# Kernel tuning notes

Measured on AMD Instinct MI355X. Metric: run time of the kernel, lower is better.

The kernel has to match this reference:

```python
import jax, jax.numpy as jnp
import numpy as np

D_MODEL = 512; DEPTH = 4; HEADS = 8; BUCKET = 256; N_HASHES = 4
INPUT_DIM = 32; SEQ = 2 * BUCKET; BATCH = 16; DH = D_MODEL // HEADS
N_BUCKETS = SEQ // BUCKET  # 2 (seq_len is forced to 2*bucket_size by pos_encoding)
SELF_ATTN_VALUE = -5e4  # TOKEN_SELF_ATTN_VALUE in reformer_pytorch


def layer_norm(x, g, b, eps=1e-5):
    m = jnp.mean(x, -1, keepdims=True)
    v = jnp.mean((x - m) ** 2, -1, keepdims=True)
    return (x - m) / jnp.sqrt(v + eps) * g + b


def look_one_back(x):
    # each chunk also attends to the previous chunk (circularly)
    prev = jnp.concatenate([x[:, -1:], x[:, :-1]], axis=1)
    return jnp.concatenate([x, prev], axis=2)


def lsh_attention(qk, v, rot):
    # qk, v: (B*H, T, DH); rot: (DH, N_HASHES, N_BUCKETS//2). Shared-QK LSH attention.
    B, T, d = qk.shape
    rotated = jnp.einsum('btf,fhi->bhti', qk, rot)                  # (B, nh, T, nb/2)
    rotated = jnp.concatenate([rotated, -rotated], axis=-1)        # (B, nh, T, nb)
    buckets = jnp.argmax(rotated, axis=-1)                          # (B, nh, T)
    offsets = (jnp.arange(N_HASHES) * N_BUCKETS)[None, :, None]
    buckets = (buckets + offsets).reshape(B, N_HASHES * T)
    ticker = jnp.arange(N_HASHES * T) % T
    bkt = T * buckets + ticker[None, :]                             # unique sort keys
    sticker = jnp.argsort(bkt, axis=-1)
    undo = jnp.argsort(sticker, axis=-1)
    st = sticker % T
    sqk = jnp.take_along_axis(qk, st[..., None], axis=1)            # (B, nh*T, d)
    sv = jnp.take_along_axis(v, st[..., None], axis=1)
    nch = N_HASHES * N_BUCKETS
    bq_t = st.reshape(B, nch, -1)
    bqk = sqk.reshape(B, nch, -1, d)
    bv = sv.reshape(B, nch, -1, d)
    bq = bqk
    bk = bqk / jnp.maximum(jnp.linalg.norm(bqk, axis=-1, keepdims=True), 1e-12)
    bk = look_one_back(bk)
    bv = look_one_back(bv)
    bkv_t = look_one_back(bq_t[..., None])[..., 0]
    dots = jnp.einsum('bcie,bcje->bcij', bq, bk) * (d ** -0.5)      # (B, nch, c, 2c)
    neg = -jnp.finfo(dots.dtype).max
    dots = jnp.where(bq_t[:, :, :, None] < bkv_t[:, :, None, :], neg, dots)   # causal
    dots = jnp.where(bq_t[:, :, :, None] == bkv_t[:, :, None, :], SELF_ATTN_VALUE, dots)  # de-prioritize self
    lse = jax.scipy.special.logsumexp(dots, axis=-1, keepdims=True)
    p = jnp.exp(dots - lse)
    bo = jnp.einsum('bcij,bcje->bcie', p, bv)
    so = bo.reshape(B, N_HASHES * T, d)
    sl = lse.reshape(B, N_HASHES * T)
    o = jnp.take_along_axis(so, undo[..., None], axis=1).reshape(B, N_HASHES, T, d)
    lg = jnp.take_along_axis(sl, undo, axis=1).reshape(B, N_HASHES, T, 1)
    w = jnp.exp(lg - jax.scipy.special.logsumexp(lg, axis=1, keepdims=True))  # combine hash rounds
    return jnp.sum(o * w, axis=1)


def lsh_self_attn(x, wqk, wv, wo, wo_b, rot):
    b, t, dm = x.shape
    split = lambda z: z.reshape(b, t, HEADS, DH).transpose(0, 2, 1, 3).reshape(b * HEADS, t, DH)
    o = lsh_attention(split(x @ wqk), split(x @ wv), rot)
    o = o.reshape(b, HEADS, t, DH).transpose(0, 2, 1, 3).reshape(b, t, dm)
    return o @ wo + wo_b


def setup_inputs() -> dict:
    key = jax.random.key(0)
    ks = jax.random.split(key, 12)
    f = lambda k, shape: jax.random.normal(k, shape, jnp.float32) * 0.02
    D, DEP, FF = D_MODEL, DEPTH, 4 * D_MODEL
    return {
        'x': jax.random.normal(ks[0], (BATCH, SEQ, INPUT_DIM), jnp.float32),
        'emb_w': f(ks[1], (INPUT_DIM, D)), 'emb_b': jnp.zeros((D,), jnp.float32),
        'pos': f(ks[2], (1, SEQ, D)),
        'ln1_g': jnp.ones((DEP, D), jnp.float32), 'ln1_b': jnp.zeros((DEP, D), jnp.float32),
        'wqk': f(ks[3], (DEP, D, D)), 'wv': f(ks[4], (DEP, D, D)),
        'wo': f(ks[5], (DEP, D, D)), 'wo_b': jnp.zeros((DEP, D), jnp.float32),
        'ln2_g': jnp.ones((DEP, D), jnp.float32), 'ln2_b': jnp.zeros((DEP, D), jnp.float32),
        'ff_w1': f(ks[6], (DEP, D, FF)), 'ff_b1': jnp.zeros((DEP, FF), jnp.float32),
        'ff_w2': f(ks[7], (DEP, FF, D)), 'ff_b2': jnp.zeros((DEP, D), jnp.float32),
        'rot': jax.random.normal(ks[8], (DEP, DH, N_HASHES, N_BUCKETS // 2), jnp.float32),
        'lnf_g': jnp.ones((D,), jnp.float32), 'lnf_b': jnp.zeros((D,), jnp.float32),
        'hw1': f(ks[9], (D, D // 2)), 'hb1': jnp.zeros((D // 2,), jnp.float32),
        'hln_g': jnp.ones((D // 2,), jnp.float32), 'hln_b': jnp.zeros((D // 2,), jnp.float32),
        'hw2': f(ks[10], (D // 2, 1)), 'hb2': jnp.zeros((1,), jnp.float32),
    }


def reference(x, emb_w, emb_b, pos, ln1_g, ln1_b, wqk, wv, wo, wo_b, ln2_g, ln2_b,
              ff_w1, ff_b1, ff_w2, ff_b2, rot, lnf_g, lnf_b, hw1, hb1, hln_g, hln_b, hw2, hb2):
    h = x @ emb_w + emb_b + pos
    # reversible residual stack (forward math): x1 += attn(norm(x2)); x2 += ff(norm(x1))
    x1 = h
    x2 = h
    for i in range(DEPTH):
        x1 = x1 + lsh_self_attn(layer_norm(x2, ln1_g[i], ln1_b[i]), wqk[i], wv[i], wo[i], wo_b[i], rot[i])
        hn = layer_norm(x1, ln2_g[i], ln2_b[i])
        x2 = x2 + jax.nn.gelu(hn @ ff_w1[i] + ff_b1[i], approximate=False) @ ff_w2[i] + ff_b2[i]
    h = 0.5 * (x1 + x2)
    h = layer_norm(h, lnf_g, lnf_b)[:, -1, :]
    h = jax.nn.relu(layer_norm(h @ hw1 + hb1, hln_g, hln_b))
    return h @ hw2 + hb2
```

## Files before the change

kernel.cpp:

```cpp
#include <hip/hip_runtime.h>
#include <hip/hip_fp16.h>
#include <cfloat>
#include <cstdint>

#define BB      16
#define TT      512
#define DD      512
#define HH      8
#define DHH     64
#define FFD     2048
#define BHH     128
#define NHASH   4
#define NCHUNK  8
#define CHUNKSZ 256
#define NLAYER  4

typedef unsigned short u16;
typedef unsigned int   u32;
typedef __attribute__((ext_vector_type(8))) short bfrag;
typedef __attribute__((ext_vector_type(4))) float f4x;
typedef __attribute__((ext_vector_type(16))) float f16x;

union FragU { u32 u[4]; uint4 v4; bfrag f; };

__device__ __forceinline__ unsigned pk_bf16(float a, float b) {
    union { float f; unsigned u; } x, y;
    x.f = a; y.f = b;
    unsigned lo = ((x.u + 0x7FFFu + ((x.u >> 16) & 1u)) >> 16) & 0xFFFFu;
    unsigned hi = (y.u + 0x7FFFu + ((y.u >> 16) & 1u)) & 0xFFFF0000u;
    return lo | hi;
}
__device__ __forceinline__ unsigned cvt_pk(float a, float b) {
    unsigned r;
    asm("v_cvt_pk_bf16_f32 %0, %1, %2" : "=v"(r) : "v"(a), "v"(b));
    return r;
}
__device__ __forceinline__ unsigned pkrtz(float a, float b) {
    unsigned r;
    asm("v_cvt_pkrtz_f16_f32 %0, %1, %2" : "=v"(r) : "v"(a), "v"(b));
    return r;
}
__device__ __forceinline__ u16 bf16_1(float a) {
    union { float f; unsigned u; } x; x.f = a;
    return (u16)((x.u + 0x7FFFu + ((x.u >> 16) & 1u)) >> 16);
}
__device__ __forceinline__ float b2f(u16 h) {
    union { unsigned u; float f; } x; x.u = ((unsigned)h) << 16; return x.f;
}

__device__ __forceinline__ void gload16(const u16* g, u16* l) {
    __builtin_amdgcn_global_load_lds(
        (const __attribute__((address_space(1))) u32*)g,
        (__attribute__((address_space(3))) u32*)l, 16, 0, 0);
}

__global__ __launch_bounds__(256)
void embed_kernel(const float* __restrict__ x, const float* __restrict__ ew,
                  const float* __restrict__ eb, const float* __restrict__ pos,
                  float* __restrict__ x1, float* __restrict__ x2)
{
    const int row = blockIdx.x;
    const int t = row & (TT - 1);
    __shared__ float xr[32];
    if (threadIdx.x < 32) xr[threadIdx.x] = x[row * 32 + threadIdx.x];
    __syncthreads();
    for (int d = threadIdx.x; d < DD; d += 256) {
        float s = eb[d] + pos[t * DD + d];
        #pragma unroll
        for (int k = 0; k < 32; ++k) s = fmaf(xr[k], ew[k * DD + d], s);
        x1[(size_t)row * DD + d] = s;
        x2[(size_t)row * DD + d] = s;
    }
}

__global__ __launch_bounds__(256)
void ln_kernel(const float* __restrict__ in, const float* __restrict__ g,
               const float* __restrict__ bta, float* __restrict__ out,
               u16* __restrict__ outh)
{
    const int row = blockIdx.x * 4 + (threadIdx.x >> 6);
    const int lane = threadIdx.x & 63;
    const float* r = in + (size_t)row * DD;
    float vals[8];
    float s = 0.0f;
    #pragma unroll
    for (int i = 0; i < 8; ++i) { vals[i] = r[i * 64 + lane]; s += vals[i]; }
    #pragma unroll
    for (int o = 1; o < 64; o <<= 1) s += __shfl_xor(s, o);
    const float mean = s * (1.0f / 512.0f);
    float vs = 0.0f;
    #pragma unroll
    for (int i = 0; i < 8; ++i) { float d = vals[i] - mean; vs += d * d; }
    #pragma unroll
    for (int o = 1; o < 64; o <<= 1) vs += __shfl_xor(vs, o);
    const float rstd = rsqrtf(vs * (1.0f / 512.0f) + 1e-5f);
    u16* hrow = outh + (size_t)row * DD;
    #pragma unroll
    for (int i = 0; i < 8; ++i) {
        const int d = i * 64 + lane;
        const float y = (vals[i] - mean) * rstd * g[d] + bta[d];
        if (out != nullptr) out[(size_t)row * DD + d] = y;
        hrow[d] = bf16_1(y);
    }
}

__global__ __launch_bounds__(256)
void prep_weights(const float* __restrict__ wqk, const float* __restrict__ wv,
                  const float* __restrict__ wo, const float* __restrict__ ffw1,
                  const float* __restrict__ ffw2,
                  u16* __restrict__ wqkvT, u16* __restrict__ woT,
                  u16* __restrict__ w1T, u16* __restrict__ w2T)
{
    const int id = blockIdx.x;
    const float* in; u16* outp; int K, N, kt, nt;
    if (id < 3072) {
        const int fam = id >> 10;
        const int r = id & 1023;
        const int L = r >> 8, t = r & 255;
        K = 512; N = 512;
        const size_t off = (size_t)L * 512 * 512;
        in = (fam == 0 ? wqk : fam == 1 ? wv : wo) + off;
        outp = (fam == 2) ? (woT + off)
                          : (wqkvT + (size_t)L * 1024 * 512 + (fam == 1 ? (size_t)512 * 512 : 0));
        kt = (t & 15) << 5; nt = (t >> 4) << 5;
    } else if (id < 7168) {
        const int r = id - 3072;
        const int L = r >> 10, t = r & 1023;
        K = 512; N = 2048;
        in = ffw1 + (size_t)L * 512 * 2048;
        outp = w1T + (size_t)L * 2048 * 512;
        kt = (t & 15) << 5; nt = (t >> 4) << 5;
    } else {
        const int r = id - 7168;
        const int L = r >> 10, t = r & 1023;
        K = 2048; N = 512;
        in = ffw2 + (size_t)L * 2048 * 512;
        outp = w2T + (size_t)L * 512 * 2048;
        kt = (t & 63) << 5; nt = (t >> 6) << 5;
    }
    __shared__ float tile[32][33];
    const int rr = threadIdx.x >> 3, c4 = (threadIdx.x & 7) * 4;
    const float4 v4 = *(const float4*)(in + (size_t)(kt + rr) * N + nt + c4);
    tile[rr][c4 + 0] = v4.x; tile[rr][c4 + 1] = v4.y;
    tile[rr][c4 + 2] = v4.z; tile[rr][c4 + 3] = v4.w;
    __syncthreads();
    uint2 p;
    p.x = pk_bf16(tile[c4 + 0][rr], tile[c4 + 1][rr]);
    p.y = pk_bf16(tile[c4 + 2][rr], tile[c4 + 3][rr]);
    *(uint2*)(outp + (size_t)(nt + rr) * K + kt + c4) = p;
}

__global__ __launch_bounds__(256)
void wrot_kernel(const float* __restrict__ wqk, const float* __restrict__ rot,
                 float* __restrict__ wrotAll)
{
    const int hh = blockIdx.x, L = blockIdx.y;
    const int head = hh >> 2, h = hh & 3;
    __shared__ float rc[64];
    if (threadIdx.x < 64)
        rc[threadIdx.x] = rot[((size_t)L * 64 + threadIdx.x) * 4 + h];
    __syncthreads();
    for (int f = threadIdx.x; f < 512; f += 256) {
        const float* wrow = wqk + (size_t)L * 512 * 512 + (size_t)f * 512 + head * 64;
        float s = 0.0f;
        #pragma unroll
        for (int d = 0; d < 64; d += 4) {
            const float4 w4 = *(const float4*)(wrow + d);
            s += w4.x * rc[d] + w4.y * rc[d + 1] + w4.z * rc[d + 2] + w4.w * rc[d + 3];
        }
        wrotAll[((size_t)L * 512 + f) * 32 + hh] = s;
    }
}

__global__ __launch_bounds__(256)
void rot_gemm(const float* __restrict__ A, const float* __restrict__ Wr,
              float* __restrict__ C)
{
    __shared__ float As[64][36];
    __shared__ float Ws[32][36];
    const int m0 = blockIdx.x * 64;
    const int r = threadIdx.x >> 2, cg = threadIdx.x & 3;
    float acc[8] = {};
    for (int f0 = 0; f0 < 512; f0 += 32) {
        __syncthreads();
        {
            const int lr = threadIdx.x >> 2, lc = (threadIdx.x & 3) * 8;
            const float* ap = A + (size_t)(m0 + lr) * 512 + f0 + lc;
            *(float4*)&As[lr][lc]     = ((const float4*)ap)[0];
            *(float4*)&As[lr][lc + 4] = ((const float4*)ap)[1];
            const int wr = threadIdx.x >> 3, wc = (threadIdx.x & 7) * 4;
            *(float4*)&Ws[wr][wc] = *(const float4*)(Wr + (size_t)(f0 + wr) * 32 + wc);
        }
        __syncthreads();
        #pragma unroll
        for (int kk = 0; kk < 32; ++kk) {
            const float a = As[r][kk];
            #pragma unroll
            for (int c = 0; c < 8; ++c)
                acc[c] = fmaf(a, Ws[kk][cg * 8 + c], acc[c]);
        }
    }
    float* crow = C + (size_t)(m0 + r) * 32 + cg * 8;
    *(float4*)crow       = make_float4(acc[0], acc[1], acc[2], acc[3]);
    *(float4*)(crow + 4) = make_float4(acc[4], acc[5], acc[6], acc[7]);
}

__device__ __forceinline__ float gelu1(float v) {
    return 0.5f * v * (1.0f + erff(v * 0.70710678118654752440f));
}
__device__ __forceinline__ int swz_row(int r, int BK) {
    return (BK == 32) ? ((r & 3) ^ ((r >> 2) & 3)) : (r & 7);
}

template<int BM, int BN, int BK, bool GELU, bool ADD, bool BIAS, bool OUTBF, bool QKV>
__global__ __launch_bounds__(256)
void gemm_bf16(const u16* __restrict__ A, const u16* __restrict__ WT,
               const float* __restrict__ bias, const float* __restrict__ addsrc,
               float* __restrict__ Cf, u16* __restrict__ Cb,
               int M, int N, int K)
{
    constexpr int NCH = BK / 8;
    constexpr int CPA = BM * NCH / 256;
    constexpr int CPB = BN * NCH / 256;
    constexpr int MR = BM / 32, NR = BN / 32, KR = BK / 32;
    __shared__ __align__(16) u16 Abuf[2][BM * BK];
    __shared__ __align__(16) u16 Bbuf[2][BN * BK];
    const int tid = threadIdx.x;
    const int m0 = blockIdx.x * BM, n0 = blockIdx.y * BN;

    const u16* aSrc[CPA]; const u16* bSrc[CPB];
    #pragma unroll
    for (int i = 0; i < CPA; ++i) {
        const int s = tid + i * 256, row = s / NCH, ch = s % NCH;
        aSrc[i] = A + (size_t)(m0 + row) * K + (ch ^ swz_row(row, BK)) * 8;
    }
    #pragma unroll
    for (int i = 0; i < CPB; ++i) {
        const int s = tid + i * 256, row = s / NCH, ch = s % NCH;
        bSrc[i] = WT + (size_t)(n0 + row) * K + (ch ^ swz_row(row, BK)) * 8;
    }

    auto STAGE = [&](int bufi, int koff) {
        #pragma unroll
        for (int i = 0; i < CPA; ++i)
            gload16(aSrc[i] + koff, &Abuf[bufi][(tid + i * 256) * 8]);
        #pragma unroll
        for (int i = 0; i < CPB; ++i)
            gload16(bSrc[i] + koff, &Bbuf[bufi][(tid + i * 256) * 8]);
    };

    const int l = tid & 63, wv_ = tid >> 6;
    const int wm = (wv_ >> 1) * (BM / 2);
    const int wn = (wv_ & 1) * (BN / 2);
    const int fr = l & 15, fc = l >> 4;

    f4x acc[MR][NR] = {};
    const int nK = K / BK;
    STAGE(0, 0);
    for (int ks = 0; ks < nK; ++ks) {
        __syncthreads();
        if (ks + 1 < nK) STAGE((ks + 1) & 1, (ks + 1) * BK);
        const u16* Ab = Abuf[ks & 1];
        const u16* Bb = Bbuf[ks & 1];
        FragU af[MR][KR], bf_[NR][KR];
        #pragma unroll
        for (int i = 0; i < MR; ++i)
            #pragma unroll
            for (int u = 0; u < KR; ++u) {
                const int r = wm + i * 16 + fr;
                af[i][u].v4 = *(const uint4*)((const char*)Ab +
                    (size_t)r * (2 * BK) + (((u * 4 + fc) ^ swz_row(r, BK)) << 4));
            }
        #pragma unroll
        for (int j = 0; j < NR; ++j)
            #pragma unroll
            for (int u = 0; u < KR; ++u) {
                const int r = wn + j * 16 + fr;
                bf_[j][u].v4 = *(const uint4*)((const char*)Bb +
                    (size_t)r * (2 * BK) + (((u * 4 + fc) ^ swz_row(r, BK)) << 4));
            }
        #pragma unroll
        for (int u = 0; u < KR; ++u)
            #pragma unroll
            for (int i = 0; i < MR; ++i)
                #pragma unroll
                for (int j = 0; j < NR; ++j)
                    acc[i][j] = __builtin_amdgcn_mfma_f32_16x16x32_bf16(
                        af[i][u].f, bf_[j][u].f, acc[i][j], 0, 0, 0);
    }

    #pragma unroll
    for (int i = 0; i < MR; ++i) {
        #pragma unroll
        for (int q = 0; q < 4; ++q) {
            const int row = m0 + wm + i * 16 + fc * 4 + q;
            #pragma unroll
            for (int j = 0; j < NR; ++j) {
                const int col = n0 + wn + j * 16 + fr;
                float vx = acc[i][j][q];
                if constexpr (BIAS) vx += bias[col];
                if constexpr (GELU) vx = gelu1(vx);
                if constexpr (ADD) vx += addsrc[(size_t)row * N + col];
                if constexpr (QKV) {
                    if (n0 < 512) {
                        const int bq = row >> 9, tq = row & 511;
                        const int hq = col >> 6, dq = col & 63;
                        Cb[(((size_t)(bq * 8 + hq) * 512) + tq) * 64 + dq] = bf16_1(vx);
                    } else {
                        ((u16*)Cf)[(size_t)row * 512 + (col - 512)] = bf16_1(vx);
                    }
                } else if constexpr (OUTBF) {
                    Cb[(size_t)row * N + col] = bf16_1(vx);
                } else {
                    Cf[(size_t)row * N + col] = vx;
                }
            }
        }
    }
}

__global__ __launch_bounds__(256)
void knorm_kernel(const u16* __restrict__ qkh, u16* __restrict__ qkn,
                  float* __restrict__ qnrm)
{
    const int g = blockIdx.x * 16 + (threadIdx.x >> 4);
    const int li = threadIdx.x & 15;
    const uint2 raw = *(const uint2*)(qkh + (size_t)g * 64 + li * 4);
    const float v0 = b2f((u16)(raw.x & 0xffff)), v1 = b2f((u16)(raw.x >> 16));
    const float v2 = b2f((u16)(raw.y & 0xffff)), v3 = b2f((u16)(raw.y >> 16));
    float ss = v0 * v0 + v1 * v1 + v2 * v2 + v3 * v3;
    ss += __shfl_xor(ss, 1); ss += __shfl_xor(ss, 2);
    ss += __shfl_xor(ss, 4); ss += __shfl_xor(ss, 8);
    const float qn = sqrtf(ss);
    const float rv = 1.0f / fmaxf(qn, 1e-12f);
    uint2 o;
    o.x = cvt_pk(v0 * rv, v1 * rv);
    o.y = cvt_pk(v2 * rv, v3 * rv);
    *(uint2*)(qkn + (size_t)g * 64 + li * 4) = o;
    if (li == 0) qnrm[g] = qn;
}

__global__ __launch_bounds__(512)
void bucket_sort_kernel(const float* __restrict__ rotated, int* __restrict__ st)
{
    const int h = blockIdx.x, bh = blockIdx.y;
    const int b = bh >> 3, head = bh & 7;
    const int t = threadIdx.x;
    __shared__ int zcnt[8];
    const float r = rotated[((size_t)(b * TT + t)) * 32 + head * 4 + h];
    const int bit = (r < 0.0f) ? 1 : 0;
    const int wid = t >> 6, lane = t & 63;
    const unsigned long long zm = __ballot(bit == 0);
    if (lane == 0) zcnt[wid] = __popcll(zm);
    __syncthreads();
    int zoff = 0, Z = 0;
    #pragma unroll
    for (int w = 0; w < 8; ++w) { const int cn = zcnt[w]; if (w < wid) zoff += cn; Z += cn; }
    const int zpre = __popcll(zm & ((1ull << lane) - 1ull));
    const int dst = (bit == 0) ? (zoff + zpre)
                               : (Z + (wid * 64 - zoff) + (lane - zpre));
    st[((size_t)bh * NHASH + h) * TT + dst] = t;
}

__global__ __launch_bounds__(512, 4)
void lsh_attn_mfma(const u16* __restrict__ qkn, const u16* __restrict__ v,
                   const float* __restrict__ qnrm, const int* __restrict__ st,
                   __half* __restrict__ o_hash, float* __restrict__ lse_hash)
{
    const int cc = blockIdx.x, bh = blockIdx.y;
    const int b = bh >> 3, head = bh & 7;
    const int h = cc >> 1, c = cc & 1;
    const int pcc = (cc + 7) & 7;
    const int hp = pcc >> 1, cp = pcc & 1;
    const int tid = threadIdx.x;
    const int w = tid >> 6;
    const int lane = tid & 63;
    const int l31 = lane & 31;
    const int hi = lane >> 5;
    const int* stb = st + (size_t)bh * (NHASH * TT);
    const size_t vbase = ((size_t)b * TT) * DD + head * DHH;
    const u16* qknb = qkn + (size_t)bh * TT * DHH;

    __shared__ __align__(16) u16 Kbf[2][64 * 64];
    __shared__ __align__(16) u16 VTbf[2][64 * 64];
    __shared__ __align__(16) int ktl[2][64];

    const int q_t = stb[h * TT + c * CHUNKSZ + w * 32 + l31];
    const float qn = qnrm[(size_t)bh * TT + q_t];
    const float mnat = qn * 0.125f;
    const float aC = qn * 0.1803368801111137f;
    uint4 QF4[4];
    {
        const u16* qrow = qknb + (size_t)q_t * DHH;
        #pragma unroll
        for (int ds = 0; ds < 4; ++ds)
            QF4[ds] = *(const uint4*)(qrow + ds * 16 + hi * 8);
    }

    f16x acc[2] = {};
    float lacc = 0.f;
    const int k8 = tid >> 3;
    const int c8 = tid & 7;
    const int brc = ((c8 & 1) << 2) | (c8 & 2) | ((c8 & 4) >> 2);
    const int wSlot = ((k8 >> 3) + brc) & 7;
    const int g2 = l31 >> 3;
    const int brg = ((g2 & 1) << 2) | (g2 & 2);

    auto gather = [&](int t8, uint4& kc, uint4& vc, int& ktc) {
        const int kj = t8 * 64 + k8;
        const int k_t = (kj < CHUNKSZ) ? stb[h * TT + c * CHUNKSZ + kj]
                                       : stb[hp * TT + cp * CHUNKSZ + (kj - CHUNKSZ)];
        ktc = k_t;
        kc = *(const uint4*)(qknb + (size_t)k_t * DHH + c8 * 8);
        vc = *(const uint4*)(v + vbase + (size_t)k_t * DD + c8 * 8);
    };
    auto writeTile = [&](int bi, const uint4& kc, const uint4& vc, int ktc) {
        *(uint4*)((char*)Kbf[bi] + ((k8 * 128 + c8 * 16) ^ ((k8 & 7) << 4))) = kc;
        const unsigned vu[4] = {vc.x, vc.y, vc.z, vc.w};
        #pragma unroll
        for (int i = 0; i < 8; ++i) {
            const int d = c8 * 8 + i;
            const u16 hv = (u16)((i & 1) ? (vu[i >> 1] >> 16) : (vu[i >> 1] & 0xffff));
            *(u16*)((char*)VTbf[bi] + d * 128 + wSlot * 16 + (k8 & 7) * 2) = hv;
        }
        if (c8 == 0) ktl[bi][k8] = ktc;
    };

    uint4 kc, vc; int ktc;
    gather(0, kc, vc, ktc);
    writeTile(0, kc, vc, ktc);
    __syncthreads();

    for (int kt8 = 0; kt8 < 8; ++kt8) {
        const int cur = kt8 & 1;
        if (kt8 < 7) gather(kt8 + 1, kc, vc, ktc);
        const u16* Kb = Kbf[cur];
        const u16* Vb = VTbf[cur];
        const int* kl = ktl[cur];

        #pragma unroll
        for (int kt = 0; kt < 2; ++kt) {
            int4 kt4[4];
            #pragma unroll
            for (int j = 0; j < 4; ++j)
                kt4[j] = *(const int4*)&kl[kt * 32 + 8 * j + 4 * hi];
            const int* ktvp = (const int*)kt4;
            FragU KA[4];
            #pragma unroll
            for (int ds = 0; ds < 4; ++ds) {
                const int row = kt * 32 + l31;
                KA[ds].v4 = *(const uint4*)((const char*)Kb +
                    ((row * 128 + ds * 32 + hi * 16) ^ ((row & 7) << 4)));
            }
            FragU VA[2][2];
            #pragma unroll
            for (int dt = 0; dt < 2; ++dt)
                #pragma unroll
                for (int u = 0; u < 2; ++u) {
                    const int row = dt * 32 + l31;
                    const int cr = (kt * 2 + u) * 2 + hi;
                    const int slot = (cr + brg + dt) & 7;
                    VA[dt][u].v4 = *(const uint4*)((const char*)Vb +
                        row * 128 + slot * 16);
                }
            f16x s = {0.f,0.f,0.f,0.f,0.f,0.f,0.f,0.f,
                      0.f,0.f,0.f,0.f,0.f,0.f,0.f,0.f};
            #pragma unroll
            for (int ds = 0; ds < 4; ++ds) {
                FragU qf; qf.v4 = QF4[ds];
                s = __builtin_amdgcn_mfma_f32_32x32x16_bf16(KA[ds].f, qf.f, s, 0, 0, 0);
            }
            float pv[16];
            #pragma unroll
            for (int i = 0; i < 16; ++i) {
                const float e = exp2f(fmaf(s[i], aC, -aC));
                const float p = (q_t > ktvp[i]) ? e : 0.0f;
                pv[i] = p;
                lacc += p;
            }
            unsigned P2[8];
            #pragma unroll
            for (int g = 0; g < 4; ++g) {
                P2[2*g]   = cvt_pk(pv[4*g],   pv[4*g+1]);
                P2[2*g+1] = cvt_pk(pv[4*g+2], pv[4*g+3]);
            }
            #pragma unroll
            for (int u = 0; u < 2; ++u) {
                unsigned a0 = P2[4*u + 0], b0 = P2[4*u + 2];
                unsigned a1 = P2[4*u + 1], b1 = P2[4*u + 3];
                asm("v_permlane32_swap_b32 %0, %1" : "+v"(a0), "+v"(b0));
                asm("v_permlane32_swap_b32 %0, %1" : "+v"(a1), "+v"(b1));
                FragU bfv;
                bfv.u[0] = a0; bfv.u[1] = a1; bfv.u[2] = b0; bfv.u[3] = b1;
                #pragma unroll
                for (int dt = 0; dt < 2; ++dt)
                    acc[dt] = __builtin_amdgcn_mfma_f32_32x32x16_bf16(
                        VA[dt][u].f, bfv.f, acc[dt], 0, 0, 0);
            }
        }

        if (kt8 < 7) {
            writeTile(cur ^ 1, kc, vc, ktc);
            __syncthreads();
        }
    }

    const float lt = lacc + __shfl_xor(lacc, 32);
    const float invl = (lt > 0.f) ? 1.0f / lt : 0.0f;
    if (hi == 0) {
        const float lse = (lt > 0.f) ? (mnat + logf(lt)) : -5.0e4f;
        lse_hash[(size_t)(bh * NHASH + h) * TT + q_t] = lse;
    }
    unsigned wa[8], wb[8];
    #pragma unroll
    for (int m = 0; m < 8; ++m) {
        wa[m] = pkrtz(acc[0][2*m] * invl, acc[0][2*m+1] * invl);
        wb[m] = pkrtz(acc[1][2*m] * invl, acc[1][2*m+1] * invl);
    }
    #pragma unroll
    for (int m = 0; m < 8; ++m)
        asm("v_permlane32_swap_b32 %0, %1" : "+v"(wa[m]), "+v"(wb[m]));
    __half* orow = o_hash + ((size_t)(bh * NHASH + h) * TT + q_t) * DHH + hi * 32;
    if (lt > 0.f) {
        #pragma unroll
        for (int g = 0; g < 4; ++g) {
            uint4 o;
            o.x = wa[2*g]; o.y = wa[2*g+1];
            o.z = wb[2*g]; o.w = wb[2*g+1];
            ((uint4*)orow)[g] = o;
        }
    } else {
        const u16* vr = v + vbase + (size_t)q_t * DD + hi * 32;
        #pragma unroll
        for (int g = 0; g < 4; ++g) {
            uint4 o;
            o.x = pkrtz(b2f(vr[8*g+0]), b2f(vr[8*g+1]));
            o.y = pkrtz(b2f(vr[8*g+2]), b2f(vr[8*g+3]));
            o.z = pkrtz(b2f(vr[8*g+4]), b2f(vr[8*g+5]));
            o.w = pkrtz(b2f(vr[8*g+6]), b2f(vr[8*g+7]));
            ((uint4*)orow)[g] = o;
        }
    }
}

__global__ __launch_bounds__(256)
void combine_kernel(const __half* __restrict__ o_hash, const float* __restrict__ lse_hash,
                    u16* __restrict__ am)
{
    const int idx = blockIdx.x * 4 + (threadIdx.x >> 6);
    const int lane = threadIdx.x & 63;
    const int bh = idx >> 9, t = idx & 511;
    const int b = bh >> 3, head = bh & 7;
    const float ls0 = lse_hash[(size_t)(bh * NHASH + 0) * TT + t];
    const float ls1 = lse_hash[(size_t)(bh * NHASH + 1) * TT + t];
    const float ls2 = lse_hash[(size_t)(bh * NHASH + 2) * TT + t];
    const float ls3 = lse_hash[(size_t)(bh * NHASH + 3) * TT + t];
    const float M = fmaxf(fmaxf(ls0, ls1), fmaxf(ls2, ls3));
    const float e0 = __expf(ls0 - M), e1 = __expf(ls1 - M);
    const float e2 = __expf(ls2 - M), e3 = __expf(ls3 - M);
    const float inv = 1.0f / (e0 + e1 + e2 + e3);
    const float o =
        (e0 * __half2float(o_hash[((size_t)((bh * NHASH + 0) * TT + t)) * DHH + lane]) +
         e1 * __half2float(o_hash[((size_t)((bh * NHASH + 1) * TT + t)) * DHH + lane]) +
         e2 * __half2float(o_hash[((size_t)((bh * NHASH + 2) * TT + t)) * DHH + lane]) +
         e3 * __half2float(o_hash[((size_t)((bh * NHASH + 3) * TT + t)) * DHH + lane])) * inv;
    am[((size_t)(b * TT + t)) * DD + head * DHH + lane] = bf16_1(o);
}

__device__ __forceinline__ float block_sum256(float v, volatile float* red)
{
    const int lane = threadIdx.x & 63, wid = threadIdx.x >> 6;
    #pragma unroll
    for (int o = 1; o < 64; o <<= 1) v += __shfl_xor(v, o);
    __syncthreads();
    if (lane == 0) red[wid] = v;
    __syncthreads();
    return red[0] + red[1] + red[2] + red[3];
}

__global__ __launch_bounds__(256)
void head_kernel(const float* __restrict__ x1, const float* __restrict__ x2,
                 const float* __restrict__ lnfg, const float* __restrict__ lnfb,
                 const float* __restrict__ hw1, const float* __restrict__ hb1,
                 const float* __restrict__ hlng, const float* __restrict__ hlnb,
                 const float* __restrict__ hw2, const float* __restrict__ hb2,
                 float* __restrict__ out)
{
    __shared__ float nrow[512];
    __shared__ float red[4];
    const int b = blockIdx.x, tid = threadIdx.x;
    const size_t roff = ((size_t)b * TT + (TT - 1)) * DD;
    const float v0 = 0.5f * (x1[roff + tid] + x2[roff + tid]);
    const float v1 = 0.5f * (x1[roff + 256 + tid] + x2[roff + 256 + tid]);
    const float mean = block_sum256(v0 + v1, red) * (1.0f / 512.0f);
    const float d0 = v0 - mean, d1 = v1 - mean;
    const float var = block_sum256(d0 * d0 + d1 * d1, red) * (1.0f / 512.0f);
    const float rstd = rsqrtf(var + 1e-5f);
    nrow[tid]       = d0 * rstd * lnfg[tid] + lnfb[tid];
    nrow[tid + 256] = d1 * rstd * lnfg[tid + 256] + lnfb[tid + 256];
    __syncthreads();
    float a = hb1[tid];
    for (int k = 0; k < 512; ++k) a = fmaf(nrow[k], hw1[(size_t)k * 256 + tid], a);
    const float m2 = block_sum256(a, red) * (1.0f / 256.0f);
    const float dd = a - m2;
    const float var2 = block_sum256(dd * dd, red) * (1.0f / 256.0f);
    float y = dd * rsqrtf(var2 + 1e-5f) * hlng[tid] + hlnb[tid];
    y = fmaxf(y, 0.0f);
    const float osum = block_sum256(y * hw2[tid], red);
    if (tid == 0) out[b] = osum + hb2[0];
}

extern "C" void kernel_launch(void* const* d_in, const int* in_sizes, int n_in,
                              void* d_out, int out_size, void* d_ws, size_t ws_size,
                              hipStream_t stream)
{
    (void)in_sizes; (void)n_in; (void)out_size; (void)ws_size;
    const float* x    = (const float*)d_in[0];
    const float* embw = (const float*)d_in[1];
    const float* embb = (const float*)d_in[2];
    const float* pos  = (const float*)d_in[3];
    const float* ln1g = (const float*)d_in[4];
    const float* ln1b = (const float*)d_in[5];
    const float* wqk  = (const float*)d_in[6];
    const float* wv   = (const float*)d_in[7];
    const float* wo   = (const float*)d_in[8];
    const float* wob  = (const float*)d_in[9];
    const float* ln2g = (const float*)d_in[10];
    const float* ln2b = (const float*)d_in[11];
    const float* ffw1 = (const float*)d_in[12];
    const float* ffb1 = (const float*)d_in[13];
    const float* ffw2 = (const float*)d_in[14];
    const float* ffb2 = (const float*)d_in[15];
    const float* rot  = (const float*)d_in[16];
    const float* lnfg = (const float*)d_in[17];
    const float* lnfb = (const float*)d_in[18];
    const float* hw1  = (const float*)d_in[19];
    const float* hb1  = (const float*)d_in[20];
    const float* hlng = (const float*)d_in[21];
    const float* hlnb = (const float*)d_in[22];
    const float* hw2  = (const float*)d_in[23];
    const float* hb2  = (const float*)d_in[24];
    float* out = (float*)d_out;

    const size_t SZ_BTD = (size_t)BB * TT * DD;
    const size_t SZ_OH  = (size_t)BHH * NHASH * TT * DHH;

    char* p = (char*)d_ws;
    float* x1b = (float*)p;  p += SZ_BTD * 4;
    float* x2b = (float*)p;  p += SZ_BTD * 4;
    float* xnb = (float*)p;  p += SZ_BTD * 4;
    u16*   vbh = (u16*)p;    p += SZ_BTD * 2;
    u16*   xnbh = (u16*)p;   p += SZ_BTD * 2;
    u16*   qkh  = (u16*)p;   p += SZ_BTD * 2;
    u16*   qknb = (u16*)p;   p += (size_t)BHH * TT * DHH * 2;
    float* qnrm = (float*)p; p += (size_t)BHH * TT * 4;
    float* rotated = (float*)p; p += (size_t)BB * TT * 32 * 4;
    __half* ohash = (__half*)p;
    u16*    ffmid = (u16*)p;
    p += SZ_OH * 2;
    float* lseb  = (float*)p; p += (size_t)BHH * NHASH * TT * 4;
    int*   stb   = (int*)p;   p += (size_t)BHH * NHASH * TT * 4;
    u16* wqkvT = (u16*)p; p += (size_t)NLAYER * 1024 * 512 * 2;
    u16* woT   = (u16*)p; p += (size_t)NLAYER * DD * DD * 2;
    u16* w1T   = (u16*)p; p += (size_t)NLAYER * DD * FFD * 2;
    u16* w2T   = (u16*)p; p += (size_t)NLAYER * FFD * DD * 2;
    float* wrotAll = (float*)p; p += (size_t)NLAYER * DD * 32 * 4;
    u16* amb = (u16*)xnb;

    prep_weights<<<11264, 256, 0, stream>>>(wqk, wv, wo, ffw1, ffw2,
                                            wqkvT, woT, w1T, w2T);
    wrot_kernel<<<dim3(32, NLAYER), 256, 0, stream>>>(wqk, rot, wrotAll);

    embed_kernel<<<BB * TT, 256, 0, stream>>>(x, embw, embb, pos, x1b, x2b);

    for (int L = 0; L < NLAYER; ++L) {
        const size_t w512 = (size_t)L * DD * DD;
        const size_t wff  = (size_t)L * DD * FFD;

        ln_kernel<<<2048, 256, 0, stream>>>(x2b, ln1g + L * DD, ln1b + L * DD, xnb, xnbh);
        rot_gemm<<<128, 256, 0, stream>>>(xnb, wrotAll + (size_t)L * DD * 32, rotated);
        gemm_bf16<128, 128, 32, false, false, false, false, true><<<dim3(64, 8), 256, 0, stream>>>(
            xnbh, wqkvT + (size_t)L * 1024 * 512, nullptr, nullptr,
            (float*)vbh, qkh, BB * TT, 1024, DD);
        bucket_sort_kernel<<<dim3(NHASH, BHH), 512, 0, stream>>>(rotated, stb);
        knorm_kernel<<<4096, 256, 0, stream>>>(qkh, qknb, qnrm);
        lsh_attn_mfma<<<dim3(NCHUNK, BHH), 512, 0, stream>>>(
            qknb, vbh, qnrm, stb, ohash, lseb);
        combine_kernel<<<16384, 256, 0, stream>>>(ohash, lseb, amb);
        gemm_bf16<64, 64, 64, false, true, true, false, false><<<dim3(128, 8), 256, 0, stream>>>(
            amb, woT + w512, wob + L * DD, x1b, x1b, nullptr, BB * TT, DD, DD);

        ln_kernel<<<2048, 256, 0, stream>>>(x1b, ln2g + L * DD, ln2b + L * DD, nullptr, xnbh);
        gemm_bf16<128, 128, 32, true, false, true, true, false><<<dim3(64, 16), 256, 0, stream>>>(
            xnbh, w1T + wff, ffb1 + L * FFD, nullptr, nullptr, ffmid, BB * TT, FFD, DD);
        gemm_bf16<64, 64, 64, false, true, true, false, false><<<dim3(128, 8), 256, 0, stream>>>(
            ffmid, w2T + wff, ffb2 + L * DD, x2b, x2b, nullptr, BB * TT, DD, FFD);
    }

    head_kernel<<<16, 256, 0, stream>>>(x1b, x2b, lnfg, lnfb, hw1, hb1,
                                        hlng, hlnb, hw2, hb2, out);
}
```

Measured before the change: 923.9 us.

## Fuse key normalization into QKV GEMM epilogue and retile output GEMMs

Computes the per-head L2 norm of shared QK rows inside the QKV GEMM epilogue using cross-lane shuffles, writing normalized bf16 keys and norms directly and removing the separate knorm kernel and its intermediate buffer. The attention softmax row-sum is split into two accumulators to shorten the dependency chain. The output-projection and FF2 GEMMs switch from 64x64 to 128x64 tiles with half the blocks. The fused epilogue depends on each wave covering exactly one head's 64 columns and keeps scattered scalar stores.

```diff
diff --git a/kernel.cpp b/kernel.cpp
--- a/kernel.cpp
+++ b/kernel.cpp
@@ -217,6 +217,7 @@
 void gemm_bf16(const u16* __restrict__ A, const u16* __restrict__ WT,
                const float* __restrict__ bias, const float* __restrict__ addsrc,
                float* __restrict__ Cf, u16* __restrict__ Cb,
+               float* __restrict__ qn_out,
                int M, int N, int K)
 {
     constexpr int NCH = BK / 8;
@@ -289,6 +290,47 @@
                         af[i][u].f, bf_[j][u].f, acc[i][j], 0, 0, 0);
     }
 
+    if constexpr (QKV) {
+        if (n0 < 512) {
+            const int hq = (n0 + wn) >> 6;
+            #pragma unroll
+            for (int i = 0; i < MR; ++i) {
+                #pragma unroll
+                for (int q = 0; q < 4; ++q) {
+                    const int row = m0 + wm + i * 16 + fc * 4 + q;
+                    const float v0 = acc[i][0][q], v1 = acc[i][1][q];
+                    const float v2 = acc[i][2][q], v3 = acc[i][3][q];
+                    float ss = v0 * v0 + v1 * v1 + v2 * v2 + v3 * v3;
+                    ss += __shfl_xor(ss, 1); ss += __shfl_xor(ss, 2);
+                    ss += __shfl_xor(ss, 4); ss += __shfl_xor(ss, 8);
+                    const float qnv = sqrtf(ss);
+                    const float rv = 1.0f / fmaxf(qnv, 1e-12f);
+                    const int bq = row >> 9, tq = row & 511;
+                    const size_t g = ((size_t)(bq * 8 + hq) * 512) + tq;
+                    u16* qrow = Cb + g * 64;
+                    qrow[fr]      = (u16)cvt_pk(v0 * rv, v0 * rv);
+                    qrow[16 + fr] = (u16)cvt_pk(v1 * rv, v1 * rv);
+                    qrow[32 + fr] = (u16)cvt_pk(v2 * rv, v2 * rv);
+                    qrow[48 + fr] = (u16)cvt_pk(v3 * rv, v3 * rv);
+                    if (fr == 0) qn_out[g] = qnv;
+                }
+            }
+        } else {
+            #pragma unroll
+            for (int i = 0; i < MR; ++i)
+                #pragma unroll
+                for (int q = 0; q < 4; ++q) {
+                    const int row = m0 + wm + i * 16 + fc * 4 + q;
+                    #pragma unroll
+                    for (int j = 0; j < NR; ++j) {
+                        const int col = n0 + wn + j * 16 + fr;
+                        ((u16*)Cf)[(size_t)row * 512 + (col - 512)] = bf16_1(acc[i][j][q]);
+                    }
+                }
+        }
+        return;
+    }
+
     #pragma unroll
     for (int i = 0; i < MR; ++i) {
         #pragma unroll
@@ -301,43 +343,11 @@
                 if constexpr (BIAS) vx += bias[col];
                 if constexpr (GELU) vx = gelu1(vx);
                 if constexpr (ADD) vx += addsrc[(size_t)row * N + col];
-                if constexpr (QKV) {
-                    if (n0 < 512) {
-                        const int bq = row >> 9, tq = row & 511;
-                        const int hq = col >> 6, dq = col & 63;
-                        Cb[(((size_t)(bq * 8 + hq) * 512) + tq) * 64 + dq] = bf16_1(vx);
-                    } else {
-                        ((u16*)Cf)[(size_t)row * 512 + (col - 512)] = bf16_1(vx);
-                    }
-                } else if constexpr (OUTBF) {
-                    Cb[(size_t)row * N + col] = bf16_1(vx);
-                } else {
-                    Cf[(size_t)row * N + col] = vx;
-                }
-            }
-        }
-    }
-}
-
-__global__ __launch_bounds__(256)
-void knorm_kernel(const u16* __restrict__ qkh, u16* __restrict__ qkn,
-                  float* __restrict__ qnrm)
-{
-    const int g = blockIdx.x * 16 + (threadIdx.x >> 4);
-    const int li = threadIdx.x & 15;
-    const uint2 raw = *(const uint2*)(qkh + (size_t)g * 64 + li * 4);
-    const float v0 = b2f((u16)(raw.x & 0xffff)), v1 = b2f((u16)(raw.x >> 16));
-    const float v2 = b2f((u16)(raw.y & 0xffff)), v3 = b2f((u16)(raw.y >> 16));
-    float ss = v0 * v0 + v1 * v1 + v2 * v2 + v3 * v3;
-    ss += __shfl_xor(ss, 1); ss += __shfl_xor(ss, 2);
-    ss += __shfl_xor(ss, 4); ss += __shfl_xor(ss, 8);
-    const float qn = sqrtf(ss);
-    const float rv = 1.0f / fmaxf(qn, 1e-12f);
-    uint2 o;
-    o.x = cvt_pk(v0 * rv, v1 * rv);
-    o.y = cvt_pk(v2 * rv, v3 * rv);
-    *(uint2*)(qkn + (size_t)g * 64 + li * 4) = o;
-    if (li == 0) qnrm[g] = qn;
+                if constexpr (OUTBF) Cb[(size_t)row * N + col] = bf16_1(vx);
+                else Cf[(size_t)row * N + col] = vx;
+            }
+        }
+    }
 }
 
 __global__ __launch_bounds__(512)
@@ -398,7 +408,7 @@
     }
 
     f16x acc[2] = {};
-    float lacc = 0.f;
+    float lac0 = 0.f, lac1 = 0.f;
     const int k8 = tid >> 3;
     const int c8 = tid & 7;
     const int brc = ((c8 & 1) << 2) | (c8 & 2) | ((c8 & 4) >> 2);
@@ -472,11 +482,13 @@
             }
             float pv[16];
             #pragma unroll
-            for (int i = 0; i < 16; ++i) {
-                const float e = exp2f(fmaf(s[i], aC, -aC));
-                const float p = (q_t > ktvp[i]) ? e : 0.0f;
-                pv[i] = p;
-                lacc += p;
+            for (int i = 0; i < 16; i += 2) {
+                const float e0 = exp2f(fmaf(s[i],     aC, -aC));
+                const float e1 = exp2f(fmaf(s[i + 1], aC, -aC));
+                const float p0 = (q_t > ktvp[i])     ? e0 : 0.0f;
+                const float p1 = (q_t > ktvp[i + 1]) ? e1 : 0.0f;
+                pv[i] = p0; pv[i + 1] = p1;
+                lac0 += p0; lac1 += p1;
             }
             unsigned P2[8];
             #pragma unroll
@@ -505,7 +517,8 @@
         }
     }
 
-    const float lt = lacc + __shfl_xor(lacc, 32);
+    const float lts = lac0 + lac1;
+    const float lt = lts + __shfl_xor(lts, 32);
     const float invl = (lt > 0.f) ? 1.0f / lt : 0.0f;
     if (hi == 0) {
         const float lse = (lt > 0.f) ? (mnat + logf(lt)) : -5.0e4f;
@@ -651,7 +664,6 @@
     float* xnb = (float*)p;  p += SZ_BTD * 4;
     u16*   vbh = (u16*)p;    p += SZ_BTD * 2;
     u16*   xnbh = (u16*)p;   p += SZ_BTD * 2;
-    u16*   qkh  = (u16*)p;   p += SZ_BTD * 2;
     u16*   qknb = (u16*)p;   p += (size_t)BHH * TT * DHH * 2;
     float* qnrm = (float*)p; p += (size_t)BHH * TT * 4;
     float* rotated = (float*)p; p += (size_t)BB * TT * 32 * 4;
@@ -681,20 +693,19 @@
         rot_gemm<<<128, 256, 0, stream>>>(xnb, wrotAll + (size_t)L * DD * 32, rotated);
         gemm_bf16<128, 128, 32, false, false, false, false, true><<<dim3(64, 8), 256, 0, stream>>>(
             xnbh, wqkvT + (size_t)L * 1024 * 512, nullptr, nullptr,
-            (float*)vbh, qkh, BB * TT, 1024, DD);
+            (float*)vbh, qknb, qnrm, BB * TT, 1024, DD);
         bucket_sort_kernel<<<dim3(NHASH, BHH), 512, 0, stream>>>(rotated, stb);
-        knorm_kernel<<<4096, 256, 0, stream>>>(qkh, qknb, qnrm);
         lsh_attn_mfma<<<dim3(NCHUNK, BHH), 512, 0, stream>>>(
             qknb, vbh, qnrm, stb, ohash, lseb);
         combine_kernel<<<16384, 256, 0, stream>>>(ohash, lseb, amb);
-        gemm_bf16<64, 64, 64, false, true, true, false, false><<<dim3(128, 8), 256, 0, stream>>>(
-            amb, woT + w512, wob + L * DD, x1b, x1b, nullptr, BB * TT, DD, DD);
+        gemm_bf16<128, 64, 64, false, true, true, false, false><<<dim3(64, 8), 256, 0, stream>>>(
+            amb, woT + w512, wob + L * DD, x1b, x1b, nullptr, nullptr, BB * TT, DD, DD);
 
         ln_kernel<<<2048, 256, 0, stream>>>(x1b, ln2g + L * DD, ln2b + L * DD, nullptr, xnbh);
         gemm_bf16<128, 128, 32, true, false, true, true, false><<<dim3(64, 16), 256, 0, stream>>>(
-            xnbh, w1T + wff, ffb1 + L * FFD, nullptr, nullptr, ffmid, BB * TT, FFD, DD);
-        gemm_bf16<64, 64, 64, false, true, true, false, false><<<dim3(128, 8), 256, 0, stream>>>(
-            ffmid, w2T + wff, ffb2 + L * DD, x2b, x2b, nullptr, BB * TT, DD, FFD);
+            xnbh, w1T + wff, ffb1 + L * FFD, nullptr, nullptr, ffmid, nullptr, BB * TT, FFD, DD);
+        gemm_bf16<128, 64, 64, false, true, true, false, false><<<dim3(64, 8), 256, 0, stream>>>(
+            ffmid, w2T + wff, ffb2 + L * DD, x2b, x2b, nullptr, nullptr, BB * TT, DD, FFD);
     }
 
     head_kernel<<<16, 256, 0, stream>>>(x1b, x2b, lnfg, lnfb, hw1, hb1,
```

Measured after the change: 988.4 us. 7.0% more time.
